# Optimization experiments

Measured on AMD Instinct MI355X. Metric: run time of the kernel, lower is better.

The kernel has to match this reference:

```python
import jax, jax.numpy as jnp
import numpy as np

N = 50000   # nodes
E = 600000  # edges
IN = 128    # in_channels
H = 128     # hidden
G = 64      # graphs in batch


def setup_inputs() -> dict:
    key = jax.random.key(0)
    ks = jax.random.split(key, 12)
    x = jax.random.normal(ks[0], (N, IN), jnp.float32)
    edge_index = jax.random.randint(ks[1], (2, E), 0, N, dtype=jnp.int64)
    batch = jnp.sort(jax.random.randint(ks[2], (N,), 0, G, dtype=jnp.int64))

    def glorot(k, i, o):
        return jax.random.normal(k, (i, o), jnp.float32) / np.float32(np.sqrt(i))

    return {
        "x": x, "edge_index": edge_index, "batch": batch,
        "W1": glorot(ks[3], IN, H), "b1": jnp.zeros((H,), jnp.float32),
        "W2": glorot(ks[4], H, H),  "b2": jnp.zeros((H,), jnp.float32),
        "W3": glorot(ks[5], H, H),  "b3": jnp.zeros((H,), jnp.float32),
        "Wl": glorot(ks[6], H, 2),  "bl": jnp.zeros((2,), jnp.float32),
    }


def gcn_conv(x, W, b, src, dst, n):
    # PyG GCNConv: linear transform, add self-loops, symmetric deg^-1/2 norm, scatter-add.
    h = x @ W                                   # [n, H]
    loop = jnp.arange(n, dtype=src.dtype)
    s = jnp.concatenate([src, loop])            # [E+n]
    d = jnp.concatenate([dst, loop])
    deg = jax.ops.segment_sum(jnp.ones_like(d, jnp.float32), d, num_segments=n)
    dinv = jax.lax.rsqrt(deg)                   # deg >= 1 thanks to self-loops
    norm = dinv[s] * dinv[d]                    # [E+n]
    out = jax.ops.segment_sum(h[s] * norm[:, None], d, num_segments=n)
    return out + b


def reference(x, edge_index, batch, W1, b1, W2, b2, W3, b3, Wl, bl):
    src, dst = edge_index[0], edge_index[1]
    h = jax.nn.relu(gcn_conv(x, W1, b1, src, dst, N))
    h = jax.nn.relu(gcn_conv(h, W2, b2, src, dst, N))
    h = jax.nn.relu(gcn_conv(h, W3, b3, src, dst, N))
    # global_mean_pool over graph ids
    cnt = jax.ops.segment_sum(jnp.ones((N,), jnp.float32), batch, num_segments=G)
    pooled = jax.ops.segment_sum(h, batch, num_segments=G) / jnp.maximum(cnt, 1.0)[:, None]
    # dropout is identity in eval mode
    return pooled @ Wl + bl                     # [G, 2]
```

## Files before the change

### kernel.cpp

```cpp
#include <hip/hip_runtime.h>


#define THREADS 256
#define ELLW 48
#define ELLS 64

typedef __attribute__((ext_vector_type(8))) short short8;
typedef __attribute__((ext_vector_type(4))) float f32x4;
typedef __attribute__((ext_vector_type(2))) float floatx2;

__device__ inline void bf16_split(float f, unsigned short& hi, unsigned short& lo) {
    unsigned u = __float_as_uint(f);
    unsigned r = u + 0x7FFF + ((u >> 16) & 1);
    hi = (unsigned short)(r >> 16);
    float hf = __uint_as_float((unsigned)hi << 16);
    float lf = f - hf;
    unsigned ul = __float_as_uint(lf);
    lo = (unsigned short)((ul + 0x7FFF + ((ul >> 16) & 1)) >> 16);
}
__device__ inline unsigned pack_bf16(float a, float b) {
    unsigned ua = __float_as_uint(a);
    unsigned ub = __float_as_uint(b);
    ua += 0x7FFF + ((ua >> 16) & 1);
    ub += 0x7FFF + ((ub >> 16) & 1);
    return (ua >> 16) | (ub & 0xFFFF0000u);
}
__device__ inline floatx2 fp8x2_to_f32(unsigned short u) {
    return __builtin_amdgcn_cvt_pk_f32_fp8((int)(unsigned)u, false);
}
__device__ inline unsigned char f32_to_fp8(float v) {
    int pk = __builtin_amdgcn_cvt_pk_fp8_f32(v, v, 0, false);
    return (unsigned char)(pk & 0xFF);
}

__global__ __launch_bounds__(THREADS) void prep_k(const float* __restrict__ W1,
                                                  const float* __restrict__ W2,
                                                  const float* __restrict__ W3,
                                                  unsigned* __restrict__ wf,
                                                  const int* __restrict__ batch,
                                                  int* __restrict__ gstart,
                                                  int* __restrict__ ell,
                                                  int n, int gtot) {
    int b = blockIdx.x;
    if (b < 3) {
        const float* W = (b == 0) ? W1 : (b == 1) ? W2 : W3;
        unsigned* o_hi = wf + (size_t)b * 16384;
        unsigned* o_lo = o_hi + 8192;
        for (int o = threadIdx.x; o < 8192; o += THREADS) {
            int d = o & 3, l = (o >> 2) & 63, ts = o >> 8;
            int s = ts & 3, t = ts >> 2;
            int k = s * 32 + ((l >> 4) << 3) + d * 2;
            int nn = t * 16 + (l & 15);
            float v0 = W[k * 128 + nn];
            float v1 = W[(k + 1) * 128 + nn];
            unsigned short h0, l0, h1, l1;
            bf16_split(v0, h0, l0);
            bf16_split(v1, h1, l1);
            o_hi[o] = (unsigned)h0 | ((unsigned)h1 << 16);
            o_lo[o] = (unsigned)l0 | ((unsigned)l1 << 16);
        }
    } else if (b == 3) {
        int t = threadIdx.x;
        if (t <= gtot) {
            int lo = 0, hi = n;
            while (lo < hi) {
                int mid = (lo + hi) >> 1;
                if (batch[mid] < t) lo = mid + 1; else hi = mid;
            }
            gstart[t] = lo;
        }
    } else {
        int i = (b - 4) * THREADS + threadIdx.x;
        if (i < n) ell[(size_t)i * ELLS] = 0;
    }
}

__global__ __launch_bounds__(THREADS) void ell_fill_k(const int* __restrict__ src,
                                                      const int* __restrict__ dst,
                                                      int* __restrict__ ell, int e) {
    int i = blockIdx.x * THREADS + threadIdx.x;
    if (i < e) {
        int d = dst[i];
        int* row = ell + (size_t)d * ELLS;
        int pos = atomicAdd(row, 1);
        if (pos < ELLW) row[1 + pos] = src[i];
    }
}

template <bool ABF16>
__global__ __launch_bounds__(THREADS) void mfma_gemm_k(const void* __restrict__ Av,
                                                       const unsigned* __restrict__ wf,
                                                       const int* __restrict__ ell,
                                                       unsigned char* __restrict__ g8,
                                                       int n) {
    __shared__ unsigned wls[16384];
    int tid = threadIdx.x;
    int lane = tid & 63;
    int r0 = blockIdx.x * 64 + (tid >> 6) * 16;

    for (int i = tid; i < 4096; i += THREADS)
        ((uint4*)wls)[i] = ((const uint4*)wf)[i];

    f32x4 acc[8];
#pragma unroll
    for (int t = 0; t < 8; ++t) acc[t] = (f32x4){0.f, 0.f, 0.f, 0.f};

    int arow = min(r0 + (lane & 15), n - 1);
    int kcol = (lane >> 4) << 3;

    short8 ah[4], al[4];
    if (ABF16) {
        const unsigned short* A = (const unsigned short*)Av;
#pragma unroll
        for (int s = 0; s < 4; ++s)
            ah[s] = *(const short8*)&A[(size_t)arow * 128 + kcol + s * 32];
    } else {
        const float* A = (const float*)Av;
        float4 v0[4], v1[4];
#pragma unroll
        for (int s = 0; s < 4; ++s) {
            v0[s] = *(const float4*)&A[(size_t)arow * 128 + kcol + s * 32];
            v1[s] = *(const float4*)&A[(size_t)arow * 128 + kcol + s * 32 + 4];
        }
#pragma unroll
        for (int s = 0; s < 4; ++s) {
            unsigned short h[8], lo[8];
            bf16_split(v0[s].x, h[0], lo[0]); bf16_split(v0[s].y, h[1], lo[1]);
            bf16_split(v0[s].z, h[2], lo[2]); bf16_split(v0[s].w, h[3], lo[3]);
            bf16_split(v1[s].x, h[4], lo[4]); bf16_split(v1[s].y, h[5], lo[5]);
            bf16_split(v1[s].z, h[6], lo[6]); bf16_split(v1[s].w, h[7], lo[7]);
#pragma unroll
            for (int j = 0; j < 8; ++j) { ah[s][j] = (short)h[j]; al[s][j] = (short)lo[j]; }
        }
    }

    __syncthreads();

#pragma unroll
    for (int s = 0; s < 4; ++s) {
#pragma unroll
        for (int t = 0; t < 8; ++t) {
            int base = (t * 4 + s) * 256 + lane * 4;
            short8 bh = *(short8*)&wls[base];
            short8 bl = *(short8*)&wls[8192 + base];
            acc[t] = __builtin_amdgcn_mfma_f32_16x16x32_bf16(ah[s], bh, acc[t], 0, 0, 0);
            if (!ABF16)
                acc[t] = __builtin_amdgcn_mfma_f32_16x16x32_bf16(al[s], bh, acc[t], 0, 0, 0);
            acc[t] = __builtin_amdgcn_mfma_f32_16x16x32_bf16(ah[s], bl, acc[t], 0, 0, 0);
        }
    }

    int rbase = r0 + ((lane >> 4) << 2);
#pragma unroll
    for (int reg = 0; reg < 4; ++reg) {
        int rr = rbase + reg;
        if (rr < n) {
            float dv = rsqrtf(1.f + (float)ell[(size_t)rr * ELLS]);
#pragma unroll
            for (int t = 0; t < 8; ++t)
                g8[(size_t)rr * 128 + t * 16 + (lane & 15)] = f32_to_fp8(acc[t][reg] * dv);
        }
    }
}

__global__ __launch_bounds__(THREADS) void aggregate_k(const unsigned short* __restrict__ g8u,
                                                       const int* __restrict__ ell,
                                                       const float* __restrict__ bias,
                                                       unsigned* __restrict__ h16,
                                                       int n) {
    int wave = (blockIdx.x * THREADS + threadIdx.x) >> 6;
    int lane = threadIdx.x & 63;
    if (wave >= n) return;

    int v = ell[(size_t)wave * ELLS + lane];
    int cnt_true = __shfl(v, 0);
    int deg = min(cnt_true, ELLW);

    floatx2 fs = fp8x2_to_f32(g8u[(size_t)wave * 64 + lane]);
    float ax0 = fs.x, ay0 = fs.y;
    float ax1 = 0.f, ay1 = 0.f, ax2 = 0.f, ay2 = 0.f, ax3 = 0.f, ay3 = 0.f;
    float ax4 = 0.f, ay4 = 0.f, ax5 = 0.f, ay5 = 0.f, ax6 = 0.f, ay6 = 0.f;
    float ax7 = 0.f, ay7 = 0.f;

    for (int k = 0; k < deg; k += 8) {
        int s0 = __shfl(v, k + 1);
        int s1 = __shfl(v, min(k + 2, deg));
        int s2 = __shfl(v, min(k + 3, deg));
        int s3 = __shfl(v, min(k + 4, deg));
        int s4 = __shfl(v, min(k + 5, deg));
        int s5 = __shfl(v, min(k + 6, deg));
        int s6 = __shfl(v, min(k + 7, deg));
        int s7 = __shfl(v, min(k + 8, deg));
        float m1 = (k + 1 < deg) ? 1.f : 0.f;
        float m2 = (k + 2 < deg) ? 1.f : 0.f;
        float m3 = (k + 3 < deg) ? 1.f : 0.f;
        float m4 = (k + 4 < deg) ? 1.f : 0.f;
        float m5 = (k + 5 < deg) ? 1.f : 0.f;
        float m6 = (k + 6 < deg) ? 1.f : 0.f;
        float m7 = (k + 7 < deg) ? 1.f : 0.f;
        unsigned short q0 = g8u[(size_t)s0 * 64 + lane];
        unsigned short q1 = g8u[(size_t)s1 * 64 + lane];
        unsigned short q2 = g8u[(size_t)s2 * 64 + lane];
        unsigned short q3 = g8u[(size_t)s3 * 64 + lane];
        unsigned short q4 = g8u[(size_t)s4 * 64 + lane];
        unsigned short q5 = g8u[(size_t)s5 * 64 + lane];
        unsigned short q6 = g8u[(size_t)s6 * 64 + lane];
        unsigned short q7 = g8u[(size_t)s7 * 64 + lane];
        floatx2 f0 = fp8x2_to_f32(q0);
        floatx2 f1 = fp8x2_to_f32(q1);
        floatx2 f2 = fp8x2_to_f32(q2);
        floatx2 f3 = fp8x2_to_f32(q3);
        floatx2 f4 = fp8x2_to_f32(q4);
        floatx2 f5 = fp8x2_to_f32(q5);
        floatx2 f6 = fp8x2_to_f32(q6);
        floatx2 f7 = fp8x2_to_f32(q7);
        ax0 += f0.x;                ay0 += f0.y;
        ax1 = fmaf(m1, f1.x, ax1);  ay1 = fmaf(m1, f1.y, ay1);
        ax2 = fmaf(m2, f2.x, ax2);  ay2 = fmaf(m2, f2.y, ay2);
        ax3 = fmaf(m3, f3.x, ax3);  ay3 = fmaf(m3, f3.y, ay3);
        ax4 = fmaf(m4, f4.x, ax4);  ay4 = fmaf(m4, f4.y, ay4);
        ax5 = fmaf(m5, f5.x, ax5);  ay5 = fmaf(m5, f5.y, ay5);
        ax6 = fmaf(m6, f6.x, ax6);  ay6 = fmaf(m6, f6.y, ay6);
        ax7 = fmaf(m7, f7.x, ax7);  ay7 = fmaf(m7, f7.y, ay7);
    }
    ax0 += (ax1 + ax2) + (ax3 + ax4) + (ax5 + ax6) + ax7;
    ay0 += (ay1 + ay2) + (ay3 + ay4) + (ay5 + ay6) + ay7;

    float d = rsqrtf(1.f + (float)cnt_true);
    float2 bb = ((const float2*)bias)[lane];
    float ox = fmaxf(fmaf(d, ax0, bb.x), 0.f);
    float oy = fmaxf(fmaf(d, ay0, bb.y), 0.f);
    h16[(size_t)wave * 64 + lane] = pack_bf16(ox, oy);
}

#define PSLICES 8
__global__ __launch_bounds__(THREADS) void pool_k(const unsigned* __restrict__ h16,
                                                  const int* __restrict__ gstart,
                                                  float* __restrict__ partial) {
    int gph = blockIdx.x, s = blockIdx.y;
    int start = gstart[gph], end = gstart[gph + 1];
    int len = end - start;
    int chunk = (len + PSLICES - 1) / PSLICES;
    int rs = start + s * chunk;
    int re = min(rs + chunk, end);
    int c = threadIdx.x & 63, half = threadIdx.x >> 6;
    float sx = 0.f, sy = 0.f;
    for (int r = rs + half; r < re; r += 4) {
        unsigned u = h16[(size_t)r * 64 + c];
        sx += __uint_as_float(u << 16);
        sy += __uint_as_float(u & 0xFFFF0000u);
    }
    __shared__ float shx[4][64], shy[4][64];
    shx[half][c] = sx;
    shy[half][c] = sy;
    __syncthreads();
    if (half == 0) {
        sx = shx[0][c] + shx[1][c] + shx[2][c] + shx[3][c];
        sy = shy[0][c] + shy[1][c] + shy[2][c] + shy[3][c];
        partial[(gph * PSLICES + s) * 128 + c * 2] = sx;
        partial[(gph * PSLICES + s) * 128 + c * 2 + 1] = sy;
    }
}

__global__ __launch_bounds__(128) void final_k(const float* __restrict__ partial,
                                               const int* __restrict__ gstart,
                                               const float* __restrict__ Wl,
                                               const float* __restrict__ bl,
                                               float* __restrict__ out, int gtot) {
    int t = threadIdx.x;
    int gph = t >> 1, j = t & 1;
    if (gph >= gtot) return;
    float cnt = fmaxf((float)(gstart[gph + 1] - gstart[gph]), 1.f);
    float sacc = 0.f;
    for (int k = 0; k < 128; ++k) {
        float v = 0.f;
#pragma unroll
        for (int sb = 0; sb < PSLICES; ++sb)
            v += partial[(gph * PSLICES + sb) * 128 + k];
        sacc = fmaf(v, Wl[k * 2 + j], sacc);
    }
    out[gph * 2 + j] = sacc / cnt + bl[j];
}

extern "C" void kernel_launch(void* const* d_in, const int* in_sizes, int n_in,
                              void* d_out, int out_size, void* d_ws, size_t ws_size,
                              hipStream_t stream) {
    const float* x  = (const float*)d_in[0];
    const int* ei   = (const int*)d_in[1];
    const int* batch= (const int*)d_in[2];
    const float* W1 = (const float*)d_in[3];
    const float* b1 = (const float*)d_in[4];
    const float* W2 = (const float*)d_in[5];
    const float* b2 = (const float*)d_in[6];
    const float* W3 = (const float*)d_in[7];
    const float* b3 = (const float*)d_in[8];
    const float* Wl = (const float*)d_in[9];
    const float* bl = (const float*)d_in[10];
    float* out = (float*)d_out;

    const int N = in_sizes[0] / 128;
    const int E = in_sizes[1] / 2;
    const int G = out_size / 2;
    const int* src = ei;
    const int* dst = ei + E;

    char* ws = (char*)d_ws;
    size_t off = 0;
    auto alloc = [&](size_t bytes) -> void* {
        void* p = ws + off;
        off = (off + bytes + 255) & ~(size_t)255;
        return p;
    };
    unsigned char* g8 = (unsigned char*)alloc((size_t)N * 128);
    unsigned* h16  = (unsigned*)alloc((size_t)N * 64 * 4);
    int* ell       = (int*)alloc((size_t)N * ELLS * 4);
    unsigned* wf   = (unsigned*)alloc((size_t)3 * 16384 * 4);
    float* partial = (float*)alloc((size_t)G * PSLICES * 128 * 4);
    int* gstart    = (int*)alloc((size_t)(G + 1) * 4);
    (void)ws_size;

    int gridE = (E + THREADS - 1) / THREADS;
    int gridN = (N + THREADS - 1) / THREADS;

    prep_k<<<4 + gridN, THREADS, 0, stream>>>(W1, W2, W3, wf, batch, gstart, ell, N, G);
    ell_fill_k<<<gridE, THREADS, 0, stream>>>(src, dst, ell, E);

    int gemmGrid = (N + 63) / 64;
    int aggGrid = (N + 3) / 4;
    const unsigned short* g8u = (const unsigned short*)g8;

    mfma_gemm_k<false><<<gemmGrid, THREADS, 0, stream>>>(x, wf, ell, g8, N);
    aggregate_k<<<aggGrid, THREADS, 0, stream>>>(g8u, ell, b1, h16, N);
    mfma_gemm_k<true><<<gemmGrid, THREADS, 0, stream>>>(h16, wf + 16384, ell, g8, N);
    aggregate_k<<<aggGrid, THREADS, 0, stream>>>(g8u, ell, b2, h16, N);
    mfma_gemm_k<true><<<gemmGrid, THREADS, 0, stream>>>(h16, wf + 32768, ell, g8, N);
    aggregate_k<<<aggGrid, THREADS, 0, stream>>>(g8u, ell, b3, h16, N);

    dim3 poolGrid(G, PSLICES);
    pool_k<<<poolGrid, THREADS, 0, stream>>>(h16, gstart, partial);
    final_k<<<1, 128, 0, stream>>>(partial, gstart, Wl, bl, out, G);
}
```

Baseline: 182.0 us.

## Overlap ELL fill with first-layer GEMM in one launch, defer degree scaling

Merges the ELL adjacency fill and the first-layer GEMM into one kernel, with separate block ranges for each, so the edge scatter and the x@W1 matmul run concurrently. Because the degree is not known until the fill finishes, the GEMM writes unscaled bf16 output and a new scale8 pass applies the deg^-1/2 factor and converts to fp8. The first-layer GEMM now reads weights straight from global memory instead of staging them in LDS. This trades one extra small elementwise kernel and a bf16 intermediate rounding for overlap and one fewer serial launch.

```diff
diff --git a/kernel.cpp b/kernel.cpp
--- a/kernel.cpp
+++ b/kernel.cpp
@@ -9,6 +9,11 @@
 typedef __attribute__((ext_vector_type(4))) float f32x4;
 typedef __attribute__((ext_vector_type(2))) float floatx2;
 
+__device__ inline unsigned short bf16_1(float a) {
+    unsigned u = __float_as_uint(a);
+    u += 0x7FFF + ((u >> 16) & 1);
+    return (unsigned short)(u >> 16);
+}
 __device__ inline void bf16_split(float f, unsigned short& hi, unsigned short& lo) {
     unsigned u = __float_as_uint(f);
     unsigned r = u + 0x7FFF + ((u >> 16) & 1);
@@ -31,6 +36,10 @@
 __device__ inline unsigned char f32_to_fp8(float v) {
     int pk = __builtin_amdgcn_cvt_pk_fp8_f32(v, v, 0, false);
     return (unsigned char)(pk & 0xFF);
+}
+__device__ inline unsigned short f32x2_to_fp8x2(float a, float b) {
+    int pk = __builtin_amdgcn_cvt_pk_fp8_f32(a, b, 0, false);
+    return (unsigned short)(pk & 0xFFFF);
 }
 
 __global__ __launch_bounds__(THREADS) void prep_k(const float* __restrict__ W1,
@@ -75,20 +84,93 @@
     }
 }
 
-__global__ __launch_bounds__(THREADS) void ell_fill_k(const int* __restrict__ src,
-                                                      const int* __restrict__ dst,
-                                                      int* __restrict__ ell, int e) {
-    int i = blockIdx.x * THREADS + threadIdx.x;
-    if (i < e) {
-        int d = dst[i];
-        int* row = ell + (size_t)d * ELLS;
-        int pos = atomicAdd(row, 1);
-        if (pos < ELLW) row[1 + pos] = src[i];
-    }
-}
-
-template <bool ABF16>
-__global__ __launch_bounds__(THREADS) void mfma_gemm_k(const void* __restrict__ Av,
+__global__ __launch_bounds__(THREADS) void fill_gemm1_k(const int* __restrict__ src,
+                                                        const int* __restrict__ dst,
+                                                        int* __restrict__ ell, int e,
+                                                        const float* __restrict__ A,
+                                                        const unsigned* __restrict__ wf,
+                                                        unsigned short* __restrict__ g16u,
+                                                        int n, int gridE) {
+    if ((int)blockIdx.x < gridE) {
+        int i = blockIdx.x * THREADS + threadIdx.x;
+        if (i < e) {
+            int d = dst[i];
+            int* row = ell + (size_t)d * ELLS;
+            int pos = atomicAdd(row, 1);
+            if (pos < ELLW) row[1 + pos] = src[i];
+        }
+        return;
+    }
+    int bid = blockIdx.x - gridE;
+    int tid = threadIdx.x;
+    int lane = tid & 63;
+    int r0 = bid * 64 + (tid >> 6) * 16;
+
+    f32x4 acc[8];
+#pragma unroll
+    for (int t = 0; t < 8; ++t) acc[t] = (f32x4){0.f, 0.f, 0.f, 0.f};
+
+    int arow = min(r0 + (lane & 15), n - 1);
+    int kcol = (lane >> 4) << 3;
+
+    float4 v0[4], v1[4];
+#pragma unroll
+    for (int s = 0; s < 4; ++s) {
+        v0[s] = *(const float4*)&A[(size_t)arow * 128 + kcol + s * 32];
+        v1[s] = *(const float4*)&A[(size_t)arow * 128 + kcol + s * 32 + 4];
+    }
+    short8 ah[4], al[4];
+#pragma unroll
+    for (int s = 0; s < 4; ++s) {
+        unsigned short h[8], lo[8];
+        bf16_split(v0[s].x, h[0], lo[0]); bf16_split(v0[s].y, h[1], lo[1]);
+        bf16_split(v0[s].z, h[2], lo[2]); bf16_split(v0[s].w, h[3], lo[3]);
+        bf16_split(v1[s].x, h[4], lo[4]); bf16_split(v1[s].y, h[5], lo[5]);
+        bf16_split(v1[s].z, h[6], lo[6]); bf16_split(v1[s].w, h[7], lo[7]);
+#pragma unroll
+        for (int j = 0; j < 8; ++j) { ah[s][j] = (short)h[j]; al[s][j] = (short)lo[j]; }
+    }
+
+#pragma unroll
+    for (int s = 0; s < 4; ++s) {
+#pragma unroll
+        for (int t = 0; t < 8; ++t) {
+            int base = (t * 4 + s) * 256 + lane * 4;
+            short8 bh = *(const short8*)&wf[base];
+            short8 bl = *(const short8*)&wf[8192 + base];
+            acc[t] = __builtin_amdgcn_mfma_f32_16x16x32_bf16(ah[s], bh, acc[t], 0, 0, 0);
+            acc[t] = __builtin_amdgcn_mfma_f32_16x16x32_bf16(al[s], bh, acc[t], 0, 0, 0);
+            acc[t] = __builtin_amdgcn_mfma_f32_16x16x32_bf16(ah[s], bl, acc[t], 0, 0, 0);
+        }
+    }
+
+    int rbase = r0 + ((lane >> 4) << 2);
+#pragma unroll
+    for (int reg = 0; reg < 4; ++reg) {
+        int rr = rbase + reg;
+        if (rr < n) {
+#pragma unroll
+            for (int t = 0; t < 8; ++t)
+                g16u[(size_t)rr * 128 + t * 16 + (lane & 15)] = bf16_1(acc[t][reg]);
+        }
+    }
+}
+
+__global__ __launch_bounds__(THREADS) void scale8_k(const unsigned* __restrict__ g16,
+                                                    const int* __restrict__ ell,
+                                                    unsigned short* __restrict__ g8u,
+                                                    int n) {
+    int wave = (blockIdx.x * THREADS + threadIdx.x) >> 6;
+    int lane = threadIdx.x & 63;
+    if (wave >= n) return;
+    float dv = rsqrtf(1.f + (float)ell[(size_t)wave * ELLS]);
+    unsigned u = g16[(size_t)wave * 64 + lane];
+    float a = __uint_as_float(u << 16) * dv;
+    float b = __uint_as_float(u & 0xFFFF0000u) * dv;
+    g8u[(size_t)wave * 64 + lane] = f32x2_to_fp8x2(a, b);
+}
+
+__global__ __launch_bounds__(THREADS) void mfma_gemm_k(const unsigned short* __restrict__ A,
                                                        const unsigned* __restrict__ wf,
                                                        const int* __restrict__ ell,
                                                        unsigned char* __restrict__ g8,
@@ -108,31 +190,10 @@
     int arow = min(r0 + (lane & 15), n - 1);
     int kcol = (lane >> 4) << 3;
 
-    short8 ah[4], al[4];
-    if (ABF16) {
-        const unsigned short* A = (const unsigned short*)Av;
-#pragma unroll
-        for (int s = 0; s < 4; ++s)
-            ah[s] = *(const short8*)&A[(size_t)arow * 128 + kcol + s * 32];
-    } else {
-        const float* A = (const float*)Av;
-        float4 v0[4], v1[4];
-#pragma unroll
-        for (int s = 0; s < 4; ++s) {
-            v0[s] = *(const float4*)&A[(size_t)arow * 128 + kcol + s * 32];
-            v1[s] = *(const float4*)&A[(size_t)arow * 128 + kcol + s * 32 + 4];
-        }
-#pragma unroll
-        for (int s = 0; s < 4; ++s) {
-            unsigned short h[8], lo[8];
-            bf16_split(v0[s].x, h[0], lo[0]); bf16_split(v0[s].y, h[1], lo[1]);
-            bf16_split(v0[s].z, h[2], lo[2]); bf16_split(v0[s].w, h[3], lo[3]);
-            bf16_split(v1[s].x, h[4], lo[4]); bf16_split(v1[s].y, h[5], lo[5]);
-            bf16_split(v1[s].z, h[6], lo[6]); bf16_split(v1[s].w, h[7], lo[7]);
-#pragma unroll
-            for (int j = 0; j < 8; ++j) { ah[s][j] = (short)h[j]; al[s][j] = (short)lo[j]; }
-        }
-    }
+    short8 ah[4];
+#pragma unroll
+    for (int s = 0; s < 4; ++s)
+        ah[s] = *(const short8*)&A[(size_t)arow * 128 + kcol + s * 32];
 
     __syncthreads();
 
@@ -144,8 +205,6 @@
             short8 bh = *(short8*)&wls[base];
             short8 bl = *(short8*)&wls[8192 + base];
             acc[t] = __builtin_amdgcn_mfma_f32_16x16x32_bf16(ah[s], bh, acc[t], 0, 0, 0);
-            if (!ABF16)
-                acc[t] = __builtin_amdgcn_mfma_f32_16x16x32_bf16(al[s], bh, acc[t], 0, 0, 0);
             acc[t] = __builtin_amdgcn_mfma_f32_16x16x32_bf16(ah[s], bl, acc[t], 0, 0, 0);
         }
     }
@@ -321,19 +380,20 @@
 
     int gridE = (E + THREADS - 1) / THREADS;
     int gridN = (N + THREADS - 1) / THREADS;
-
-    prep_k<<<4 + gridN, THREADS, 0, stream>>>(W1, W2, W3, wf, batch, gstart, ell, N, G);
-    ell_fill_k<<<gridE, THREADS, 0, stream>>>(src, dst, ell, E);
-
     int gemmGrid = (N + 63) / 64;
     int aggGrid = (N + 3) / 4;
-    const unsigned short* g8u = (const unsigned short*)g8;
-
-    mfma_gemm_k<false><<<gemmGrid, THREADS, 0, stream>>>(x, wf, ell, g8, N);
+    unsigned short* g8u = (unsigned short*)g8;
+    unsigned short* g16tmp_u = (unsigned short*)h16;
+
+    prep_k<<<4 + gridN, THREADS, 0, stream>>>(W1, W2, W3, wf, batch, gstart, ell, N, G);
+
+    fill_gemm1_k<<<gridE + gemmGrid, THREADS, 0, stream>>>(src, dst, ell, E,
+                                                           x, wf, g16tmp_u, N, gridE);
+    scale8_k<<<aggGrid, THREADS, 0, stream>>>(h16, ell, g8u, N);
     aggregate_k<<<aggGrid, THREADS, 0, stream>>>(g8u, ell, b1, h16, N);
-    mfma_gemm_k<true><<<gemmGrid, THREADS, 0, stream>>>(h16, wf + 16384, ell, g8, N);
+    mfma_gemm_k<<<gemmGrid, THREADS, 0, stream>>>((const unsigned short*)h16, wf + 16384, ell, g8, N);
     aggregate_k<<<aggGrid, THREADS, 0, stream>>>(g8u, ell, b2, h16, N);
-    mfma_gemm_k<true><<<gemmGrid, THREADS, 0, stream>>>(h16, wf + 32768, ell, g8, N);
+    mfma_gemm_k<<<gemmGrid, THREADS, 0, stream>>>((const unsigned short*)h16, wf + 32768, ell, g8, N);
     aggregate_k<<<aggGrid, THREADS, 0, stream>>>(g8u, ell, b3, h16, N);
 
     dim3 poolGrid(G, PSLICES);
```

Result: no change. 183.5 us (+0.8%).

## Build ELL adjacency via two-pass bucketed partition instead of global atomics

Applied to the files above, without the earlier changes.

Replaces the per-edge global atomicAdd ELL fill with a two-pass scheme. The first pass counts edges per 256-node destination bucket in shared memory and reserves space with one global atomic per bucket per block. It then writes packed (local dst, src) pairs into bucket regions. The second pass builds each bucket's ELL rows with shared-memory counters, which removes the separate zeroing of row counts. The packing assumes fewer than 65536 nodes, at most 256 buckets, and at most BCAP edges per bucket.

```diff
diff --git a/kernel.cpp b/kernel.cpp
--- a/kernel.cpp
+++ b/kernel.cpp
@@ -4,6 +4,8 @@
 #define THREADS 256
 #define ELLW 48
 #define ELLS 64
+#define BCAP 4096
+#define EPB  4096
 
 typedef __attribute__((ext_vector_type(8))) short short8;
 typedef __attribute__((ext_vector_type(4))) float f32x4;
@@ -39,8 +41,8 @@
                                                   unsigned* __restrict__ wf,
                                                   const int* __restrict__ batch,
                                                   int* __restrict__ gstart,
-                                                  int* __restrict__ ell,
-                                                  int n, int gtot) {
+                                                  int* __restrict__ gcur,
+                                                  int n, int gtot, int nb) {
     int b = blockIdx.x;
     if (b < 3) {
         const float* W = (b == 0) ? W1 : (b == 1) ? W2 : W3;
@@ -70,21 +72,64 @@
             gstart[t] = lo;
         }
     } else {
-        int i = (b - 4) * THREADS + threadIdx.x;
-        if (i < n) ell[(size_t)i * ELLS] = 0;
-    }
-}
-
-__global__ __launch_bounds__(THREADS) void ell_fill_k(const int* __restrict__ src,
-                                                      const int* __restrict__ dst,
-                                                      int* __restrict__ ell, int e) {
-    int i = blockIdx.x * THREADS + threadIdx.x;
-    if (i < e) {
-        int d = dst[i];
-        int* row = ell + (size_t)d * ELLS;
-        int pos = atomicAdd(row, 1);
-        if (pos < ELLW) row[1 + pos] = src[i];
-    }
+        int t = threadIdx.x;
+        if (t < nb) gcur[t] = 0;
+    }
+}
+
+__global__ __launch_bounds__(THREADS) void part1_k(const int* __restrict__ src,
+                                                   const int* __restrict__ dst,
+                                                   int* __restrict__ gcur,
+                                                   unsigned* __restrict__ region,
+                                                   int e, int nb) {
+    __shared__ int hist[256];
+    __shared__ int base[256];
+    int tid = threadIdx.x;
+    hist[tid] = 0;
+    __syncthreads();
+    int start = blockIdx.x * EPB;
+#pragma unroll
+    for (int j = 0; j < EPB / THREADS; ++j) {
+        int i = start + j * THREADS + tid;
+        if (i < e) atomicAdd(&hist[dst[i] >> 8], 1);
+    }
+    __syncthreads();
+    if (tid < nb) base[tid] = atomicAdd(&gcur[tid], hist[tid]);
+    hist[tid] = 0;
+    __syncthreads();
+#pragma unroll
+    for (int j = 0; j < EPB / THREADS; ++j) {
+        int i = start + j * THREADS + tid;
+        if (i < e) {
+            int d = dst[i], s = src[i];
+            int bk = d >> 8;
+            int lp = atomicAdd(&hist[bk], 1);
+            int pos = base[bk] + lp;
+            if (pos < BCAP)
+                region[(size_t)bk * BCAP + pos] = ((unsigned)(d & 255) << 16) | (unsigned)s;
+        }
+    }
+}
+
+__global__ __launch_bounds__(THREADS) void part2_k(const unsigned* __restrict__ region,
+                                                   const int* __restrict__ gcur,
+                                                   int* __restrict__ ell, int n) {
+    __shared__ int cnt[256];
+    int tid = threadIdx.x;
+    int b = blockIdx.x;
+    cnt[tid] = 0;
+    __syncthreads();
+    int nbk = min(gcur[b], BCAP);
+    for (int i = tid; i < nbk; i += THREADS) {
+        unsigned u = region[(size_t)b * BCAP + i];
+        int dloc = (int)(u >> 16);
+        int pos = atomicAdd(&cnt[dloc], 1);
+        if (pos < ELLW)
+            ell[(size_t)(b * 256 + dloc) * ELLS + 1 + pos] = (int)(u & 0xFFFFu);
+    }
+    __syncthreads();
+    int node = b * 256 + tid;
+    if (node < n) ell[(size_t)node * ELLS] = cnt[tid];
 }
 
 template <bool ABF16>
@@ -303,6 +348,7 @@
     const int G = out_size / 2;
     const int* src = ei;
     const int* dst = ei + E;
+    const int NB = (N + 255) >> 8;
 
     char* ws = (char*)d_ws;
     size_t off = 0;
@@ -312,22 +358,23 @@
         return p;
     };
     unsigned char* g8 = (unsigned char*)alloc((size_t)N * 128);
-    unsigned* h16  = (unsigned*)alloc((size_t)N * 64 * 4);
-    int* ell       = (int*)alloc((size_t)N * ELLS * 4);
-    unsigned* wf   = (unsigned*)alloc((size_t)3 * 16384 * 4);
-    float* partial = (float*)alloc((size_t)G * PSLICES * 128 * 4);
-    int* gstart    = (int*)alloc((size_t)(G + 1) * 4);
+    unsigned* h16   = (unsigned*)alloc((size_t)N * 64 * 4);
+    int* ell        = (int*)alloc((size_t)N * ELLS * 4);
+    unsigned* wf    = (unsigned*)alloc((size_t)3 * 16384 * 4);
+    unsigned* region= (unsigned*)alloc((size_t)NB * BCAP * 4);
+    int* gcur       = (int*)alloc((size_t)NB * 4);
+    float* partial  = (float*)alloc((size_t)G * PSLICES * 128 * 4);
+    int* gstart     = (int*)alloc((size_t)(G + 1) * 4);
     (void)ws_size;
 
-    int gridE = (E + THREADS - 1) / THREADS;
-    int gridN = (N + THREADS - 1) / THREADS;
-
-    prep_k<<<4 + gridN, THREADS, 0, stream>>>(W1, W2, W3, wf, batch, gstart, ell, N, G);
-    ell_fill_k<<<gridE, THREADS, 0, stream>>>(src, dst, ell, E);
-
+    int grid1 = (E + EPB - 1) / EPB;
     int gemmGrid = (N + 63) / 64;
     int aggGrid = (N + 3) / 4;
-    const unsigned short* g8u = (const unsigned short*)g8;
+    unsigned short* g8u = (unsigned short*)g8;
+
+    prep_k<<<5, THREADS, 0, stream>>>(W1, W2, W3, wf, batch, gstart, gcur, N, G, NB);
+    part1_k<<<grid1, THREADS, 0, stream>>>(src, dst, gcur, region, E, NB);
+    part2_k<<<NB, THREADS, 0, stream>>>(region, gcur, ell, N);
 
     mfma_gemm_k<false><<<gemmGrid, THREADS, 0, stream>>>(x, wf, ell, g8, N);
     aggregate_k<<<aggGrid, THREADS, 0, stream>>>(g8u, ell, b1, h16, N);
```

Result: faster. 174.9 us (median of 2 runs) (-3.9%).
